# Kernel tuning notes

Measured on AMD Instinct MI355X. Metric: run time of the kernel, lower is better.

The kernel has to match this reference:

```python
import jax, jax.numpy as jnp
import numpy as np
from jax import lax

SIGMA = 4.0
RADIUS = int(4.0 * SIGMA + 0.5)  # scipy gaussian_filter default truncate=4.0 -> radius 16


def _gaussian_kernel1d(sigma, radius):
    x = jnp.arange(-radius, radius + 1, dtype=jnp.float32)
    phi = jnp.exp(-0.5 * (x / sigma) ** 2)
    return phi / phi.sum()


def _gaussian_blur(img):
    # img: [B, H, W]; scipy mode='reflect' == numpy pad mode='symmetric'
    k = _gaussian_kernel1d(SIGMA, RADIUS)
    K = 2 * RADIUS + 1
    x = jnp.pad(img, ((0, 0), (RADIUS, RADIUS), (RADIUS, RADIUS)), mode='symmetric')[:, None]  # [B,1,H+2r,W+2r]
    x = lax.conv_general_dilated(x, k.reshape(1, 1, K, 1), (1, 1), 'VALID')  # blur rows
    x = lax.conv_general_dilated(x, k.reshape(1, 1, 1, K), (1, 1), 'VALID')  # blur cols
    return x[:, 0]


def setup_inputs() -> dict:
    key = jax.random.key(0)
    k1, k2, k3 = jax.random.split(key, 3)
    B, C, P, h, w, crop = 16, 256, 3136, 56, 56, 224
    embeddings = jax.random.normal(k1, (B, C, P), dtype=jnp.float32)
    means = jax.random.normal(k2, (P, C), dtype=jnp.float32) * 0.1
    # SPD inverse covariance: I + low-rank, so the quadratic form is positive (sqrt-safe)
    u = jax.random.normal(k3, (P, C, 4), dtype=jnp.float32) * 0.1
    inv_cov = jnp.einsum('pcr,pdr->pcd', u, u) + jnp.eye(C, dtype=jnp.float32)
    return {"embeddings": embeddings, "means": means, "inv_cov": inv_cov,
            "h": h, "w": w, "crop_size": crop}


def reference(embeddings, means, inv_cov, h, w, crop_size):
    # embeddings: [B, C, P], means: [P, C], inv_cov: [P, C, C]
    b = embeddings.shape[0]
    delta = jnp.transpose(embeddings, (0, 2, 1)) - means[None]           # [B, P, C]
    d2 = jnp.einsum('bpc,pcd,bpd->bp', delta, inv_cov, delta)            # Mahalanobis^2
    dist = jnp.sqrt(d2).reshape(b, h, w)
    # F.interpolate(mode='bilinear', align_corners=False) == jax.image.resize bilinear (upsampling)
    score = jax.image.resize(dist, (b, crop_size, crop_size), method='bilinear')
    score = _gaussian_blur(score)
    mn, mx = score.min(), score.max()
    return (score - mn) / (mx - mn)
```

## Files before the change

kernel.cpp:

```cpp
#include <hip/hip_runtime.h>
#include <math.h>

#define NP 3136
#define NC 256
#define NB 16
#define HH 56
#define OW 224

__device__ __forceinline__ void rowstep(const float4 mv, const int c,
                                        const float (&dreg)[4][16], float (&z)[16],
                                        const float (*dc_lds)[20]) {
  float s[16];
#pragma unroll
  for (int b = 0; b < 16; ++b) s[b] = mv.x * dreg[0][b];
#pragma unroll
  for (int b = 0; b < 16; ++b) s[b] = fmaf(mv.y, dreg[1][b], s[b]);
#pragma unroll
  for (int b = 0; b < 16; ++b) s[b] = fmaf(mv.z, dreg[2][b], s[b]);
#pragma unroll
  for (int b = 0; b < 16; ++b) s[b] = fmaf(mv.w, dreg[3][b], s[b]);
#pragma unroll
  for (int q = 0; q < 4; ++q) {
    const float4 dc = *reinterpret_cast<const float4*>(&dc_lds[c][4 * q]);
    z[4 * q + 0] = fmaf(dc.x, s[4 * q + 0], z[4 * q + 0]);
    z[4 * q + 1] = fmaf(dc.y, s[4 * q + 1], z[4 * q + 1]);
    z[4 * q + 2] = fmaf(dc.z, s[4 * q + 2], z[4 * q + 2]);
    z[4 * q + 3] = fmaf(dc.w, s[4 * q + 3], z[4 * q + 3]);
  }
}

__global__ __launch_bounds__(256) void k_dist(const float* __restrict__ emb,
                                              const float* __restrict__ means,
                                              const float* __restrict__ icov,
                                              float* __restrict__ dist,
                                              unsigned int* __restrict__ mm) {
  __shared__ float dc_lds[NC][20];
  __shared__ float db_lds[NB][NC + 8];
  __shared__ float zbuf[4][16];

  const int bid = blockIdx.x;
  const int p = (bid & 7) * (NP >> 3) + (bid >> 3);
  const int t = threadIdx.x;
  const int lane = t & 63;
  const int wv = t >> 6;

  if (bid == 0 && t == 0) {
    mm[0] = 0x7f800000u;
    mm[1] = 0u;
    mm[2] = 0u;
  }

  {
    const int c = t;
    const float mn = means[(size_t)p * NC + c];
    const float* ep = emb + (size_t)c * NP + p;
    float d[16];
#pragma unroll
    for (int b = 0; b < 16; ++b) d[b] = ep[(size_t)b * (NC * NP)] - mn;
#pragma unroll
    for (int q = 0; q < 4; ++q) {
      *reinterpret_cast<float4*>(&dc_lds[c][4 * q]) =
          make_float4(d[4 * q], d[4 * q + 1], d[4 * q + 2], d[4 * q + 3]);
    }
#pragma unroll
    for (int b = 0; b < 16; ++b) db_lds[b][c] = d[b];
  }
  __syncthreads();

  float dreg[4][16];
#pragma unroll
  for (int b = 0; b < 16; ++b) {
    const float4 v = *reinterpret_cast<const float4*>(&db_lds[b][4 * lane]);
    dreg[0][b] = v.x; dreg[1][b] = v.y; dreg[2][b] = v.z; dreg[3][b] = v.w;
  }

  float z[16];
#pragma unroll
  for (int b = 0; b < 16; ++b) z[b] = 0.f;

  const float* mbase = icov + (size_t)p * (NC * NC) + (size_t)(wv * 64) * NC + 4 * lane;
#define LOADM(r) (*reinterpret_cast<const float4*>(mbase + (size_t)(r) * NC))

  float4 m0 = LOADM(0), m1 = LOADM(1), m2 = LOADM(2), m3 = LOADM(3);
  for (int rb = 0; rb < 64; rb += 4) {
    const int r4 = (rb + 4 < 64) ? rb + 4 : 63;
    const int r5 = (rb + 5 < 64) ? rb + 5 : 63;
    const int r6 = (rb + 6 < 64) ? rb + 6 : 63;
    const int r7 = (rb + 7 < 64) ? rb + 7 : 63;
    const float4 n0 = LOADM(r4);
    const float4 n1 = LOADM(r5);
    const float4 n2 = LOADM(r6);
    const float4 n3 = LOADM(r7);
    rowstep(m0, wv * 64 + rb + 0, dreg, z, dc_lds);
    rowstep(m1, wv * 64 + rb + 1, dreg, z, dc_lds);
    rowstep(m2, wv * 64 + rb + 2, dreg, z, dc_lds);
    rowstep(m3, wv * 64 + rb + 3, dreg, z, dc_lds);
    m0 = n0; m1 = n1; m2 = n2; m3 = n3;
  }
#undef LOADM

#pragma unroll
  for (int b = 0; b < 16; ++b) {
    float v = z[b];
#pragma unroll
    for (int off = 32; off > 0; off >>= 1) v += __shfl_xor(v, off, 64);
    z[b] = v;
  }
  if (lane == 0) {
#pragma unroll
    for (int b = 0; b < 16; ++b) zbuf[wv][b] = z[b];
  }
  __syncthreads();
  if (t < 16) {
    const float d2 = zbuf[0][t] + zbuf[1][t] + zbuf[2][t] + zbuf[3][t];
    dist[(size_t)t * NP + p] = sqrtf(d2);
  }
}

__global__ __launch_bounds__(256) void k_blur(const float* __restrict__ dist,
                                              float* __restrict__ out,
                                              unsigned int* __restrict__ mm) {
  __shared__ float w[33];
  __shared__ float ld[56 * 56];
  __shared__ float ccx[56][13];
  __shared__ float ccy[224][13];
  __shared__ int xlo[56];
  __shared__ int ylo[224];
  __shared__ float rb[56][57];
  __shared__ float sout[224][56];
  __shared__ float red[4][2];

  const int t = threadIdx.x;
  const int b = blockIdx.x >> 2;
  const int x0 = (blockIdx.x & 3) * 56;

  if (t < 33) {
    const float d = (float)(t - 16);
    w[t] = expf(-d * d * (1.f / 32.f));
  }
  for (int i = t; i < 56 * 56; i += 256) ld[i] = dist[(size_t)b * NP + i];
  __syncthreads();

  if (t < 224) {
    const int y = t;
    int lo = 56;
    for (int j = 0; j < 33; ++j) {
      int yy = y + j - 16;
      yy = (yy < 0) ? (-1 - yy) : (yy >= 224 ? 447 - yy : yy);
      const int U = (int)floorf(yy * 0.25f - 0.375f);
      const int u0c = U < 0 ? 0 : U;
      lo = lo < u0c ? lo : u0c;
    }
    ylo[y] = lo;
#pragma unroll
    for (int n = 0; n < 13; ++n) ccy[y][n] = 0.f;
    for (int j = 0; j < 33; ++j) {
      int yy = y + j - 16;
      yy = (yy < 0) ? (-1 - yy) : (yy >= 224 ? 447 - yy : yy);
      const float sy = yy * 0.25f - 0.375f;
      const int U = (int)floorf(sy);
      const float fy = sy - (float)U;
      const int u0c = U < 0 ? 0 : U;
      const int u1c = (U + 1) > 55 ? 55 : (U + 1);
      ccy[y][u0c - lo] += w[j] * (1.f - fy);
      ccy[y][u1c - lo] += w[j] * fy;
    }
  }
  if (t < 56) {
    const int x = x0 + t;
    int lo = 56;
    for (int j = 0; j < 33; ++j) {
      int xx = x + j - 16;
      xx = (xx < 0) ? (-1 - xx) : (xx >= 224 ? 447 - xx : xx);
      const int U = (int)floorf(xx * 0.25f - 0.375f);
      const int u0c = U < 0 ? 0 : U;
      lo = lo < u0c ? lo : u0c;
    }
    xlo[t] = lo;
#pragma unroll
    for (int n = 0; n < 13; ++n) ccx[t][n] = 0.f;
    for (int j = 0; j < 33; ++j) {
      int xx = x + j - 16;
      xx = (xx < 0) ? (-1 - xx) : (xx >= 224 ? 447 - xx : xx);
      const float sx = xx * 0.25f - 0.375f;
      const int U = (int)floorf(sx);
      const float fx = sx - (float)U;
      const int u0c = U < 0 ? 0 : U;
      const int u1c = (U + 1) > 55 ? 55 : (U + 1);
      ccx[t][u0c - lo] += w[j] * (1.f - fx);
      ccx[t][u1c - lo] += w[j] * fx;
    }
  }
  __syncthreads();

  for (int i = t; i < 56 * 56; i += 256) {
    const int u = i / 56, lx = i - 56 * u;
    const int lo = xlo[lx];
    const float* lrow = &ld[u * 56];
    float acc = 0.f;
#pragma unroll
    for (int n = 0; n < 13; ++n) {
      int v = lo + n;
      v = v > 55 ? 55 : v;
      acc = fmaf(ccx[lx][n], lrow[v], acc);
    }
    rb[u][lx] = acc;
  }
  __syncthreads();

  float mnv = 1e30f, mxv = 0.f;
  if (t < 224) {
    const int y = t;
    const int lo = ylo[y];
    for (int c = 0; c < 7; ++c) {
      float a0 = 0.f, a1 = 0.f, a2 = 0.f, a3 = 0.f,
            a4 = 0.f, a5 = 0.f, a6 = 0.f, a7 = 0.f;
#pragma unroll
      for (int n = 0; n < 13; ++n) {
        int u = lo + n;
        u = u > 55 ? 55 : u;
        const float cy = ccy[y][n];
        const float* rrow = &rb[u][c * 8];
        a0 = fmaf(cy, rrow[0], a0); a1 = fmaf(cy, rrow[1], a1);
        a2 = fmaf(cy, rrow[2], a2); a3 = fmaf(cy, rrow[3], a3);
        a4 = fmaf(cy, rrow[4], a4); a5 = fmaf(cy, rrow[5], a5);
        a6 = fmaf(cy, rrow[6], a6); a7 = fmaf(cy, rrow[7], a7);
      }
      float* srow = &sout[y][c * 8];
      srow[0] = a0; srow[1] = a1; srow[2] = a2; srow[3] = a3;
      srow[4] = a4; srow[5] = a5; srow[6] = a6; srow[7] = a7;
      mnv = fminf(mnv, fminf(fminf(fminf(a0, a1), fminf(a2, a3)),
                             fminf(fminf(a4, a5), fminf(a6, a7))));
      mxv = fmaxf(mxv, fmaxf(fmaxf(fmaxf(a0, a1), fmaxf(a2, a3)),
                             fmaxf(fmaxf(a4, a5), fmaxf(a6, a7))));
    }
  }
#pragma unroll
  for (int off = 32; off > 0; off >>= 1) {
    mnv = fminf(mnv, __shfl_xor(mnv, off, 64));
    mxv = fmaxf(mxv, __shfl_xor(mxv, off, 64));
  }
  const int lane = t & 63, wv = t >> 6;
  if (lane == 0) { red[wv][0] = mnv; red[wv][1] = mxv; }
  __syncthreads();

  if (t == 0) {
    const float m0 = fminf(fminf(red[0][0], red[1][0]), fminf(red[2][0], red[3][0]));
    const float m1 = fmaxf(fmaxf(red[0][1], red[1][1]), fmaxf(red[2][1], red[3][1]));
    atomicMin(&mm[0], __float_as_uint(m0));
    atomicMax(&mm[1], __float_as_uint(m1));
    __threadfence();
    atomicAdd(&mm[2], 1u);
    while (atomicAdd(&mm[2], 0u) < 64u) {
    }
    __threadfence();
    red[0][0] = __uint_as_float(atomicAdd(&mm[0], 0u));
    red[0][1] = __uint_as_float(atomicAdd(&mm[1], 0u));
  }
  __syncthreads();

  const float gmn = red[0][0];
  const float inv = 1.f / (red[0][1] - gmn);
  for (int i = t; i < 224 * 14; i += 256) {
    const int y = i / 14, c = i - 14 * y;
    const float* s = &sout[y][c * 4];
    float4 v = make_float4((s[0] - gmn) * inv, (s[1] - gmn) * inv,
                           (s[2] - gmn) * inv, (s[3] - gmn) * inv);
    *reinterpret_cast<float4*>(out + ((size_t)b * OW + y) * OW + x0 + c * 4) = v;
  }
}

extern "C" void kernel_launch(void* const* d_in, const int* in_sizes, int n_in,
                              void* d_out, int out_size, void* d_ws, size_t ws_size,
                              hipStream_t stream) {
  const float* emb = (const float*)d_in[0];
  const float* means = (const float*)d_in[1];
  const float* icov = (const float*)d_in[2];
  float* out = (float*)d_out;

  char* ws = (char*)d_ws;
  float* dist = (float*)ws;
  unsigned int* mm = (unsigned int*)(ws + 3416064);

  k_dist<<<NP, 256, 0, stream>>>(emb, means, icov, dist, mm);
  k_blur<<<NB * 4, 256, 0, stream>>>(dist, out, mm);
}
```

Baseline: 207.1 us.

## Use nontemporal inv_cov loads issued early and split blur into y-halves

The distance kernel now issues the first inverse-covariance loads before the delta/LDS setup and makes them nontemporal, so streaming the 822MB matrix overlaps with setup and does not pollute the cache. The blur kernel splits each column tile into two row halves, doubling the block count to 128. Each block now computes only the 33 horizontally blurred rows it needs and uses a 2-thread-per-row vertical pass. The grid-wide min/max barrier is raised to 128 blocks, which relies on all blocks being co-resident.

```diff
diff --git a/kernel.cpp b/kernel.cpp
--- a/kernel.cpp
+++ b/kernel.cpp
@@ -7,18 +7,20 @@
 #define HH 56
 #define OW 224
 
-__device__ __forceinline__ void rowstep(const float4 mv, const int c,
+typedef float f4 __attribute__((ext_vector_type(4)));
+
+__device__ __forceinline__ void rowstep(const f4 mv, const int c,
                                         const float (&dreg)[4][16], float (&z)[16],
                                         const float (*dc_lds)[20]) {
   float s[16];
 #pragma unroll
-  for (int b = 0; b < 16; ++b) s[b] = mv.x * dreg[0][b];
-#pragma unroll
-  for (int b = 0; b < 16; ++b) s[b] = fmaf(mv.y, dreg[1][b], s[b]);
-#pragma unroll
-  for (int b = 0; b < 16; ++b) s[b] = fmaf(mv.z, dreg[2][b], s[b]);
-#pragma unroll
-  for (int b = 0; b < 16; ++b) s[b] = fmaf(mv.w, dreg[3][b], s[b]);
+  for (int b = 0; b < 16; ++b) s[b] = mv[0] * dreg[0][b];
+#pragma unroll
+  for (int b = 0; b < 16; ++b) s[b] = fmaf(mv[1], dreg[1][b], s[b]);
+#pragma unroll
+  for (int b = 0; b < 16; ++b) s[b] = fmaf(mv[2], dreg[2][b], s[b]);
+#pragma unroll
+  for (int b = 0; b < 16; ++b) s[b] = fmaf(mv[3], dreg[3][b], s[b]);
 #pragma unroll
   for (int q = 0; q < 4; ++q) {
     const float4 dc = *reinterpret_cast<const float4*>(&dc_lds[c][4 * q]);
@@ -50,6 +52,12 @@
     mm[2] = 0u;
   }
 
+  const float* mbase = icov + (size_t)p * (NC * NC) + (size_t)(wv * 64) * NC + 4 * lane;
+#define LOADM(r) __builtin_nontemporal_load( \
+    reinterpret_cast<const f4*>(mbase + (size_t)(r) * NC))
+
+  f4 m0 = LOADM(0), m1 = LOADM(1), m2 = LOADM(2), m3 = LOADM(3);
+
   {
     const int c = t;
     const float mn = means[(size_t)p * NC + c];
@@ -78,19 +86,15 @@
 #pragma unroll
   for (int b = 0; b < 16; ++b) z[b] = 0.f;
 
-  const float* mbase = icov + (size_t)p * (NC * NC) + (size_t)(wv * 64) * NC + 4 * lane;
-#define LOADM(r) (*reinterpret_cast<const float4*>(mbase + (size_t)(r) * NC))
-
-  float4 m0 = LOADM(0), m1 = LOADM(1), m2 = LOADM(2), m3 = LOADM(3);
   for (int rb = 0; rb < 64; rb += 4) {
     const int r4 = (rb + 4 < 64) ? rb + 4 : 63;
     const int r5 = (rb + 5 < 64) ? rb + 5 : 63;
     const int r6 = (rb + 6 < 64) ? rb + 6 : 63;
     const int r7 = (rb + 7 < 64) ? rb + 7 : 63;
-    const float4 n0 = LOADM(r4);
-    const float4 n1 = LOADM(r5);
-    const float4 n2 = LOADM(r6);
-    const float4 n3 = LOADM(r7);
+    const f4 n0 = LOADM(r4);
+    const f4 n1 = LOADM(r5);
+    const f4 n2 = LOADM(r6);
+    const f4 n3 = LOADM(r7);
     rowstep(m0, wv * 64 + rb + 0, dreg, z, dc_lds);
     rowstep(m1, wv * 64 + rb + 1, dreg, z, dc_lds);
     rowstep(m2, wv * 64 + rb + 2, dreg, z, dc_lds);
@@ -123,16 +127,19 @@
   __shared__ float w[33];
   __shared__ float ld[56 * 56];
   __shared__ float ccx[56][13];
-  __shared__ float ccy[224][13];
+  __shared__ float ccy[112][13];
   __shared__ int xlo[56];
-  __shared__ int ylo[224];
-  __shared__ float rb[56][57];
-  __shared__ float sout[224][56];
+  __shared__ int ylo[112];
+  __shared__ float rbuf[33][57];
+  __shared__ float sout[112][56];
   __shared__ float red[4][2];
 
   const int t = threadIdx.x;
-  const int b = blockIdx.x >> 2;
-  const int x0 = (blockIdx.x & 3) * 56;
+  const int b = blockIdx.x >> 3;
+  const int x0 = ((blockIdx.x >> 1) & 3) * 56;
+  const int yh = blockIdx.x & 1;
+  const int ybase = yh * 112;
+  const int ubase = yh * 23;
 
   if (t < 33) {
     const float d = (float)(t - 16);
@@ -141,8 +148,8 @@
   for (int i = t; i < 56 * 56; i += 256) ld[i] = dist[(size_t)b * NP + i];
   __syncthreads();
 
-  if (t < 224) {
-    const int y = t;
+  if (t < 112) {
+    const int y = ybase + t;
     int lo = 56;
     for (int j = 0; j < 33; ++j) {
       int yy = y + j - 16;
@@ -151,9 +158,9 @@
       const int u0c = U < 0 ? 0 : U;
       lo = lo < u0c ? lo : u0c;
     }
-    ylo[y] = lo;
-#pragma unroll
-    for (int n = 0; n < 13; ++n) ccy[y][n] = 0.f;
+    ylo[t] = lo;
+#pragma unroll
+    for (int n = 0; n < 13; ++n) ccy[t][n] = 0.f;
     for (int j = 0; j < 33; ++j) {
       int yy = y + j - 16;
       yy = (yy < 0) ? (-1 - yy) : (yy >= 224 ? 447 - yy : yy);
@@ -162,8 +169,8 @@
       const float fy = sy - (float)U;
       const int u0c = U < 0 ? 0 : U;
       const int u1c = (U + 1) > 55 ? 55 : (U + 1);
-      ccy[y][u0c - lo] += w[j] * (1.f - fy);
-      ccy[y][u1c - lo] += w[j] * fy;
+      ccy[t][u0c - lo] += w[j] * (1.f - fy);
+      ccy[t][u1c - lo] += w[j] * fy;
     }
   }
   if (t < 56) {
@@ -193,10 +200,11 @@
   }
   __syncthreads();
 
-  for (int i = t; i < 56 * 56; i += 256) {
-    const int u = i / 56, lx = i - 56 * u;
+  for (int i = t; i < 33 * 56; i += 256) {
+    const int ur = i / 56, lx = i - 56 * ur;
+    const int u = ubase + ur;
     const int lo = xlo[lx];
-    const float* lrow = &ld[u * 56];
+    const float* lrow = &ld[(u > 55 ? 55 : u) * 56];
     float acc = 0.f;
 #pragma unroll
     for (int n = 0; n < 13; ++n) {
@@ -204,35 +212,30 @@
       v = v > 55 ? 55 : v;
       acc = fmaf(ccx[lx][n], lrow[v], acc);
     }
-    rb[u][lx] = acc;
+    rbuf[ur][lx] = acc;
   }
   __syncthreads();
 
   float mnv = 1e30f, mxv = 0.f;
   if (t < 224) {
-    const int y = t;
-    const int lo = ylo[y];
+    const int yl = t >> 1;
+    const int xh = (t & 1) * 28;
+    const int lo = ylo[yl];
     for (int c = 0; c < 7; ++c) {
-      float a0 = 0.f, a1 = 0.f, a2 = 0.f, a3 = 0.f,
-            a4 = 0.f, a5 = 0.f, a6 = 0.f, a7 = 0.f;
+      float a0 = 0.f, a1 = 0.f, a2 = 0.f, a3 = 0.f;
 #pragma unroll
       for (int n = 0; n < 13; ++n) {
-        int u = lo + n;
-        u = u > 55 ? 55 : u;
-        const float cy = ccy[y][n];
-        const float* rrow = &rb[u][c * 8];
+        int ur = lo + n - ubase;
+        ur = ur < 0 ? 0 : (ur > 32 ? 32 : ur);
+        const float cy = ccy[yl][n];
+        const float* rrow = &rbuf[ur][xh + c * 4];
         a0 = fmaf(cy, rrow[0], a0); a1 = fmaf(cy, rrow[1], a1);
         a2 = fmaf(cy, rrow[2], a2); a3 = fmaf(cy, rrow[3], a3);
-        a4 = fmaf(cy, rrow[4], a4); a5 = fmaf(cy, rrow[5], a5);
-        a6 = fmaf(cy, rrow[6], a6); a7 = fmaf(cy, rrow[7], a7);
       }
-      float* srow = &sout[y][c * 8];
+      float* srow = &sout[yl][xh + c * 4];
       srow[0] = a0; srow[1] = a1; srow[2] = a2; srow[3] = a3;
-      srow[4] = a4; srow[5] = a5; srow[6] = a6; srow[7] = a7;
-      mnv = fminf(mnv, fminf(fminf(fminf(a0, a1), fminf(a2, a3)),
-                             fminf(fminf(a4, a5), fminf(a6, a7))));
-      mxv = fmaxf(mxv, fmaxf(fmaxf(fmaxf(a0, a1), fmaxf(a2, a3)),
-                             fmaxf(fmaxf(a4, a5), fmaxf(a6, a7))));
+      mnv = fminf(mnv, fminf(fminf(a0, a1), fminf(a2, a3)));
+      mxv = fmaxf(mxv, fmaxf(fmaxf(a0, a1), fmaxf(a2, a3)));
     }
   }
 #pragma unroll
@@ -251,7 +254,7 @@
     atomicMax(&mm[1], __float_as_uint(m1));
     __threadfence();
     atomicAdd(&mm[2], 1u);
-    while (atomicAdd(&mm[2], 0u) < 64u) {
+    while (atomicAdd(&mm[2], 0u) < 128u) {
     }
     __threadfence();
     red[0][0] = __uint_as_float(atomicAdd(&mm[0], 0u));
@@ -261,12 +264,13 @@
 
   const float gmn = red[0][0];
   const float inv = 1.f / (red[0][1] - gmn);
-  for (int i = t; i < 224 * 14; i += 256) {
-    const int y = i / 14, c = i - 14 * y;
-    const float* s = &sout[y][c * 4];
+  for (int i = t; i < 112 * 14; i += 256) {
+    const int yl = i / 14, c = i - 14 * yl;
+    const float* s = &sout[yl][c * 4];
     float4 v = make_float4((s[0] - gmn) * inv, (s[1] - gmn) * inv,
                            (s[2] - gmn) * inv, (s[3] - gmn) * inv);
-    *reinterpret_cast<float4*>(out + ((size_t)b * OW + y) * OW + x0 + c * 4) = v;
+    *reinterpret_cast<float4*>(out + ((size_t)b * OW + ybase + yl) * OW + x0 +
+                               c * 4) = v;
   }
 }
 
@@ -283,5 +287,5 @@
   unsigned int* mm = (unsigned int*)(ws + 3416064);
 
   k_dist<<<NP, 256, 0, stream>>>(emb, means, icov, dist, mm);
-  k_blur<<<NB * 4, 256, 0, stream>>>(dist, out, mm);
-}
+  k_blur<<<NB * 8, 256, 0, stream>>>(dist, out, mm);
+}
```

Result: no change. 211.0 us (+1.9%).
